# Optimization experiments

Measured on AMD Instinct MI355X. Metric: run time of the kernel, lower is better.

Reference implementation:

```python
import jax, jax.numpy as jnp
import numpy as np

# Model config (matches init_kwargs)
D_MODEL = 1536
NUM_HEADS = 16
QUERY_GROUPS = 4
HEAD_DIM = D_MODEL // NUM_HEADS  # 96
HEADS_PER_GROUP = NUM_HEADS // QUERY_GROUPS
ROPE_THETA = 10000.0
B, T, GH, GW = 2, 16, 16, 16
S = GH * GW  # spatial patches per frame
QKV_OUT = NUM_HEADS * HEAD_DIM + 2 * QUERY_GROUPS * HEAD_DIM  # 2304


def setup_inputs() -> dict:
    key = jax.random.key(0)
    k1, k2, k3 = jax.random.split(key, 3)
    x = jax.random.normal(k1, (B, T, S, D_MODEL), dtype=jnp.float32)
    padding_mask = jnp.ones((B * T, S), dtype=jnp.int32)
    # nn.Linear weights stored as [out, in]; y = x @ W.T
    w_qkv = jax.random.normal(k2, (QKV_OUT, D_MODEL), dtype=jnp.float32) * (1.0 / np.sqrt(D_MODEL))
    w_o = jax.random.normal(k3, (D_MODEL, D_MODEL), dtype=jnp.float32) * (1.0 / np.sqrt(D_MODEL))
    return {"x": x, "padding_mask": padding_mask, "w_qkv": w_qkv, "w_o": w_o}


def _rot_half(seg, cos, sin):
    # seg: [..., d]; half-split rotary rotation
    d = seg.shape[-1] // 2
    x1, x2 = seg[..., :d], seg[..., d:]
    return jnp.concatenate([x1 * cos - x2 * sin, x1 * sin + x2 * cos], axis=-1)


def _cos_sin(pos, seg_dim):
    # pos: [L] -> cos/sin [L, seg_dim//2]
    inv_freq = 1.0 / (ROPE_THETA ** (jnp.arange(seg_dim // 2, dtype=jnp.float32) * 2.0 / seg_dim))
    ang = pos.astype(jnp.float32)[:, None] * inv_freq[None, :]
    return jnp.cos(ang), jnp.sin(ang)


def _apply_rope3d(x):
    # x: [B*T, S, heads, HEAD_DIM]; head_dim split equally over (t, h, w) axes
    seg = HEAD_DIM // 3  # 32
    t_pos = jnp.tile(jnp.arange(T), B)            # [B*T] temporal index per attention-batch row
    h_pos = jnp.repeat(jnp.arange(GH), GW)        # [S]
    w_pos = jnp.tile(jnp.arange(GW), GH)          # [S]
    ct, st = _cos_sin(t_pos, seg)  # [B*T, seg/2]
    ch, sh = _cos_sin(h_pos, seg)  # [S, seg/2]
    cw, sw = _cos_sin(w_pos, seg)
    xt = _rot_half(x[..., :seg], ct[:, None, None, :], st[:, None, None, :])
    xh = _rot_half(x[..., seg:2 * seg], ch[None, :, None, :], sh[None, :, None, :])
    xw = _rot_half(x[..., 2 * seg:], cw[None, :, None, :], sw[None, :, None, :])
    return jnp.concatenate([xt, xh, xw], axis=-1)


def reference(x, padding_mask, w_qkv, w_o):
    # Spatial attention mode: [B, T, S, D] -> [B*T, S, D]
    xs = x.reshape(B * T, S, D_MODEL)
    qkv = jnp.einsum('bsd,od->bso', xs, w_qkv)  # [B*T, S, QKV_OUT]
    q_end = NUM_HEADS * HEAD_DIM
    k_end = q_end + QUERY_GROUPS * HEAD_DIM
    q = qkv[..., :q_end].reshape(B * T, S, NUM_HEADS, HEAD_DIM)
    k = qkv[..., q_end:k_end].reshape(B * T, S, QUERY_GROUPS, HEAD_DIM)
    v = qkv[..., k_end:].reshape(B * T, S, QUERY_GROUPS, HEAD_DIM)
    # RoPE3D on q and k
    q = _apply_rope3d(q)
    k = _apply_rope3d(k)
    # GQA: extend kv heads to num_heads (repeat_interleave)
    k = jnp.repeat(k, HEADS_PER_GROUP, axis=2)  # [B*T, S, NUM_HEADS, HEAD_DIM]
    v = jnp.repeat(v, HEADS_PER_GROUP, axis=2)
    scale = 1.0 / np.sqrt(HEAD_DIM)
    scores = jnp.einsum('bqhd,bkhd->bhqk', q, k) * scale  # [B*T, H, S, S]
    mask = (padding_mask != 0)[:, None, None, :]  # [B*T, 1, 1, S], True = attend
    scores = jnp.where(mask, scores, jnp.float32(-1e9))
    probs = jax.nn.softmax(scores, axis=-1)
    attn = jnp.einsum('bhqk,bkhd->bqhd', probs, v).reshape(B * T, S, D_MODEL)
    out = jnp.einsum('bsd,od->bso', attn, w_o)
    return out.reshape(B, T, S, D_MODEL)
```

## Files before the change

### kernel.cpp

```cpp
#include <hip/hip_runtime.h>
#include <hip/hip_bf16.h>
#include <stdint.h>

typedef __attribute__((ext_vector_type(8))) short short8;
typedef __attribute__((ext_vector_type(4))) float f32x4;
typedef __attribute__((ext_vector_type(4))) float f4;
typedef __attribute__((ext_vector_type(4))) short s4;

typedef __attribute__((address_space(1))) const void gvoid_t;
typedef __attribute__((address_space(3))) void lvoid_t;

__device__ __forceinline__ void gload_lds16(const void* g, void* l) {
  __builtin_amdgcn_global_load_lds((gvoid_t*)g, (lvoid_t*)l, 16, 0, 0);
}

__device__ __forceinline__ ushort f2b(float f) {
  union { float f; uint32_t u; } v; v.f = f;
  return (ushort)((v.u + 0x7fffu + ((v.u >> 16) & 1u)) >> 16);
}
__device__ __forceinline__ float b2f(ushort b) {
  union { uint32_t u; float f; } v; v.u = ((uint32_t)b) << 16;
  return v.f;
}

template <int N> __device__ __forceinline__ void wait_vmcnt();
template <> __device__ __forceinline__ void wait_vmcnt<0>() { asm volatile("s_waitcnt vmcnt(0)" ::: "memory"); }

__device__ __forceinline__ void wait_lgkm0() {
  asm volatile("s_waitcnt lgkmcnt(0)" ::: "memory");
  __builtin_amdgcn_sched_barrier(0);
}

__global__ void cvt_kernel(const float* __restrict__ in, ushort* __restrict__ out, int n4) {
  int i = blockIdx.x * 256 + threadIdx.x;
  if (i < n4) {
    f4 v = ((const f4*)in)[i];
    s4 o;
    o.x = (short)f2b(v.x); o.y = (short)f2b(v.y);
    o.z = (short)f2b(v.z); o.w = (short)f2b(v.w);
    ((s4*)out)[i] = o;
  }
}

template <int BN, typename OutT>
__global__ __launch_bounds__(512, 2) void gemm6(const ushort* __restrict__ A,
                                                const ushort* __restrict__ B,
                                                OutT* __restrict__ C,
                                                int N, int K) {
  constexpr int NF = BN / 32;
  constexpr int RB = BN / 2;
  constexpr int ABUF = 256 * 64;
  constexpr int BBUF = BN * 64;
  constexpr uint ABYTE = ABUF * 2;
  constexpr uint BBYTE = BBUF * 2;
  constexpr int BRND = BN / 64;
  constexpr int BTW = (BN % 64) / 8;

  __shared__ ushort As[2 * ABUF];
  __shared__ ushort Bs[2 * BBUF];

  const int tid = threadIdx.x;
  const int l = tid & 63, w = tid >> 6;
  const int wr = w >> 1, wc = w & 1;
  const int r16 = l & 15, kh = l >> 4;
  const int sc = (l & 7) ^ (l >> 3);
  const int srow = w * 8 + (l >> 3);

  const int xcd = blockIdx.x & 7;
  const int ii = blockIdx.x >> 3;
  const int bm = xcd * 4 + (ii & 3);
  const int bn = ii >> 2;
  const ushort* Ag = A + (size_t)bm * 256 * K;
  const ushort* Bg = B + (size_t)bn * BN * K;
  const int NT = K >> 6;

  const char* AsR = (const char*)As;
  const char* BsR = (const char*)Bs;
  const uint khsw = ((uint)kh * 16) ^ ((uint)(r16 & 7) * 16);
  const uint PA = (uint)(wr * 64 + r16) * 128 + khsw;
  const uint PB = (uint)(wc * RB + r16) * 128 + khsw;

  const ushort* ga[4];
  const ushort* gb[BRND];
  const ushort* gbt = nullptr;
#pragma unroll
  for (int i = 0; i < 4; ++i) ga[i] = Ag + (size_t)(i * 64 + srow) * K + sc * 8;
#pragma unroll
  for (int i = 0; i < BRND; ++i) gb[i] = Bg + (size_t)(i * 64 + srow) * K + sc * 8;
  if constexpr (BTW > 0) gbt = Bg + (size_t)(BRND * 64 + srow) * K + sc * 8;

#pragma unroll
  for (int i = 0; i < 4; ++i) gload_lds16(ga[i], As + i * 4096 + w * 512);
#pragma unroll
  for (int i = 0; i < BRND; ++i) gload_lds16(gb[i], Bs + i * 4096 + w * 512);
  if constexpr (BTW > 0) { if (w < BTW) gload_lds16(gbt, Bs + BRND * 4096 + w * 512); }
#pragma unroll
  for (int i = 0; i < 4; ++i) ga[i] += 64;
#pragma unroll
  for (int i = 0; i < BRND; ++i) gb[i] += 64;
  if constexpr (BTW > 0) gbt += 64;
  wait_vmcnt<0>();
  __builtin_amdgcn_s_barrier();

  f32x4 acc[4][NF] = {};
  short8 afr[4], bfr[NF];

  for (int u = 0; u < NT; ++u) {
    const int cur = u & 1;
    const uint aoff = cur ? ABYTE : 0u;
    const uint boff = cur ? BBYTE : 0u;
    ushort* An = As + (cur ^ 1) * ABUF;
    ushort* Bn = Bs + (cur ^ 1) * BBUF;
    const bool st = (u + 1 < NT);

    {
      const uint pa = PA + aoff, pb = PB + boff;
#pragma unroll
      for (int m = 0; m < 4; ++m)
        afr[m] = *(const short8*)(AsR + pa + m * 2048);
#pragma unroll
      for (int n = 0; n < NF; ++n)
        bfr[n] = *(const short8*)(BsR + pb + n * 2048);
    }
    if (st) {
#pragma unroll
      for (int i = 0; i < 4; ++i) gload_lds16(ga[i], An + i * 4096 + w * 512);
    }
    wait_lgkm0();
    __builtin_amdgcn_s_setprio(1);
#pragma unroll
    for (int m = 0; m < 4; ++m)
#pragma unroll
      for (int n = 0; n < NF; ++n)
        acc[m][n] = __builtin_amdgcn_mfma_f32_16x16x32_bf16(afr[m], bfr[n], acc[m][n], 0, 0, 0);
    __builtin_amdgcn_s_setprio(0);

    {
      const uint pa = (PA ^ 64u) + aoff, pb = (PB ^ 64u) + boff;
#pragma unroll
      for (int m = 0; m < 4; ++m)
        afr[m] = *(const short8*)(AsR + pa + m * 2048);
#pragma unroll
      for (int n = 0; n < NF; ++n)
        bfr[n] = *(const short8*)(BsR + pb + n * 2048);
    }
    if (st) {
#pragma unroll
      for (int i = 0; i < BRND; ++i) gload_lds16(gb[i], Bn + i * 4096 + w * 512);
      if constexpr (BTW > 0) { if (w < BTW) gload_lds16(gbt, Bn + BRND * 4096 + w * 512); }
    }
    wait_lgkm0();
    __builtin_amdgcn_s_setprio(1);
#pragma unroll
    for (int m = 0; m < 4; ++m)
#pragma unroll
      for (int n = 0; n < NF; ++n)
        acc[m][n] = __builtin_amdgcn_mfma_f32_16x16x32_bf16(afr[m], bfr[n], acc[m][n], 0, 0, 0);
    __builtin_amdgcn_s_setprio(0);

#pragma unroll
    for (int i = 0; i < 4; ++i) ga[i] += 64;
#pragma unroll
    for (int i = 0; i < BRND; ++i) gb[i] += 64;
    if constexpr (BTW > 0) gbt += 64;
    wait_vmcnt<0>();
    __builtin_amdgcn_s_barrier();
  }

  const int rowb = bm * 256 + wr * 64;
  const int colb = bn * BN + wc * RB;
#pragma unroll
  for (int m = 0; m < 4; ++m)
#pragma unroll
    for (int n = 0; n < NF; ++n)
#pragma unroll
      for (int r = 0; r < 4; ++r) {
        int row = rowb + m * 16 + kh * 4 + r;
        int col = colb + n * 16 + r16;
        float val = acc[m][n][r];
        if constexpr (sizeof(OutT) == 2) C[(size_t)row * N + col] = f2b(val);
        else                             C[(size_t)row * N + col] = val;
      }
}

__global__ void rope_tab_kernel(float2* __restrict__ tab) {
  int t = threadIdx.x;
  int pos = t >> 4, i = t & 15;
  float inv_freq = __expf(-(float)i * 0.5756462732485115f);
  float ang = (float)pos * inv_freq;
  float sn, c;
  __sincosf(ang, &sn, &c);
  tab[t] = make_float2(c, sn);
}

__global__ void rope_kernel(const ushort* __restrict__ qkv,
                            const float2* __restrict__ tab,
                            ushort* __restrict__ Qo, ushort* __restrict__ Ko,
                            ushort* __restrict__ Vt) {
  const int UNITS = 1344;
  int idx = blockIdx.x * 256 + threadIdx.x;
  if (idx >= 8192 * UNITS) return;
  int row = idx / UNITS;
  int unit = idx - row * UNITS;
  int bt = row >> 8, s = row & 255;
  const ushort* qr = qkv + (size_t)row * 2304;
  if (unit < 960) {
    int head, p;
    size_t srcoff;
    ushort* dst;
    if (unit < 768) {
      head = unit / 48; p = unit % 48;
      srcoff = (size_t)head * 96;
      dst = Qo + ((size_t)(bt * 16 + head) * 256 + s) * 96;
    } else {
      int u = unit - 768;
      head = u / 48; p = u % 48;
      srcoff = 1536 + (size_t)head * 96;
      dst = Ko + ((size_t)(bt * 4 + head) * 256 + s) * 96;
    }
    int seg = p >> 4, i = p & 15;
    int pos = (seg == 0) ? (bt & 15) : ((seg == 1) ? (s >> 4) : (s & 15));
    float2 cs = tab[pos * 16 + i];
    float c = cs.x, sn = cs.y;
    float x1 = b2f(qr[srcoff + seg * 32 + i]);
    float x2 = b2f(qr[srcoff + seg * 32 + i + 16]);
    dst[seg * 32 + i]      = f2b(x1 * c - x2 * sn);
    dst[seg * 32 + i + 16] = f2b(x1 * sn + x2 * c);
  } else {
    int u = unit - 960;
    int g = u / 96, d = u - g * 96;
    Vt[((size_t)(bt * 4 + g) * 96 + d) * 256 + s] = qr[1920 + (size_t)g * 96 + d];
  }
}

__global__ __launch_bounds__(512, 2) void attn2_kernel(
    const ushort* __restrict__ Q,
    const ushort* __restrict__ Kr,
    const ushort* __restrict__ Vt,
    const int* __restrict__ mask,
    ushort* __restrict__ Out) {
  __shared__ ushort Ks[256 * 104];
  __shared__ ushort Vs[96 * 264];
  __shared__ ushort Ps[8][16 * 136];
  __shared__ float Mb[256];

  const int b = blockIdx.x;
  const int qt = b & 1;
  const int g = (b >> 1) & 3;
  const int bt = b >> 3;
  const int t = threadIdx.x;
  const int l = t & 63, w = t >> 6;
  const int r16 = l & 15, kh = l >> 4;
  const int h = g * 4 + (w >> 1);
  const int qc = w & 1;

  const ushort* Kp = Kr + (size_t)(bt * 4 + g) * 256 * 96;
  const ushort* Vp = Vt + (size_t)(bt * 4 + g) * 96 * 256;

  {
    int r = t >> 1, ch = t & 1;
#pragma unroll
    for (int j = 0; j < 6; ++j)
      *(short8*)(&Ks[r * 104 + ch * 48 + j * 8]) =
          *(const short8*)(Kp + (size_t)r * 96 + ch * 48 + j * 8);
  }
#pragma unroll
  for (int i = 0; i < 6; ++i) {
    int c = t + i * 512;
    int vr = c >> 5, vc = c & 31;
    *(short8*)(&Vs[vr * 264 + vc * 8]) =
        *(const short8*)(Vp + (size_t)vr * 256 + vc * 8);
  }
  if (t < 256) Mb[t] = mask[bt * 256 + t] ? 0.0f : -1.0e9f;
  __syncthreads();

  const ushort* Qp = Q + ((size_t)(bt * 16 + h) * 256 + qt * 128 + qc * 64) * 96;
  ushort* Pw = &Ps[w][0];
  const float scale = 0.10206207261596575f;

#pragma unroll
  for (int mp = 0; mp < 2; ++mp) {
    const int qb = mp * 32;

    short8 qfA[3], qfB[3];
#pragma unroll
    for (int kc = 0; kc < 3; ++kc) {
      qfA[kc] = *(const short8*)(Qp + (size_t)(qb + r16) * 96 + kc * 32 + kh * 8);
      qfB[kc] = *(const short8*)(Qp + (size_t)(qb + 16 + r16) * 96 + kc * 32 + kh * 8);
    }

    f32x4 scA[16] = {}, scB[16] = {};
#pragma unroll
    for (int f = 0; f < 16; ++f) {
#pragma unroll
      for (int kc = 0; kc < 3; ++kc) {
        short8 kf = *(const short8*)(&Ks[(f * 16 + r16) * 104 + kc * 32 + kh * 8]);
        scA[f] = __builtin_amdgcn_mfma_f32_16x16x32_bf16(qfA[kc], kf, scA[f], 0, 0, 0);
        scB[f] = __builtin_amdgcn_mfma_f32_16x16x32_bf16(qfB[kc], kf, scB[f], 0, 0, 0);
      }
    }

#pragma unroll
    for (int f = 0; f < 16; ++f) {
      float mb = Mb[f * 16 + r16];
#pragma unroll
      for (int r = 0; r < 4; ++r) {
        scA[f][r] = scA[f][r] * scale + mb;
        scB[f][r] = scB[f][r] * scale + mb;
      }
    }

    float invA[4], invB[4];
#pragma unroll
    for (int reg = 0; reg < 4; ++reg) {
      float mxA = -3.0e38f, mxB = -3.0e38f;
#pragma unroll
      for (int f = 0; f < 16; ++f) { mxA = fmaxf(mxA, scA[f][reg]); mxB = fmaxf(mxB, scB[f][reg]); }
      for (int o = 8; o >= 1; o >>= 1) { mxA = fmaxf(mxA, __shfl_xor(mxA, o, 64)); mxB = fmaxf(mxB, __shfl_xor(mxB, o, 64)); }
      float smA = 0.f, smB = 0.f;
#pragma unroll
      for (int f = 0; f < 16; ++f) {
        float pA = __expf(scA[f][reg] - mxA);
        float pB = __expf(scB[f][reg] - mxB);
        scA[f][reg] = pA; scB[f][reg] = pB;
        smA += pA; smB += pB;
      }
      for (int o = 8; o >= 1; o >>= 1) { smA += __shfl_xor(smA, o, 64); smB += __shfl_xor(smB, o, 64); }
      invA[reg] = 1.0f / smA;
      invB[reg] = 1.0f / smB;
    }

    short8 pfA[8], pfB[8];
#pragma unroll
    for (int ck = 0; ck < 2; ++ck) {
#pragma unroll
      for (int f = 0; f < 8; ++f)
#pragma unroll
        for (int reg = 0; reg < 4; ++reg)
          Pw[(kh * 4 + reg) * 136 + f * 16 + r16] = f2b(scA[ck * 8 + f][reg]);
#pragma unroll
      for (int kc = 0; kc < 4; ++kc)
        pfA[ck * 4 + kc] = *(const short8*)(&Pw[r16 * 136 + kc * 32 + kh * 8]);
    }
#pragma unroll
    for (int ck = 0; ck < 2; ++ck) {
#pragma unroll
      for (int f = 0; f < 8; ++f)
#pragma unroll
        for (int reg = 0; reg < 4; ++reg)
          Pw[(kh * 4 + reg) * 136 + f * 16 + r16] = f2b(scB[ck * 8 + f][reg]);
#pragma unroll
      for (int kc = 0; kc < 4; ++kc)
        pfB[ck * 4 + kc] = *(const short8*)(&Pw[r16 * 136 + kc * 32 + kh * 8]);
    }

    f32x4 oA[6] = {}, oB[6] = {};
#pragma unroll
    for (int dt = 0; dt < 6; ++dt) {
#pragma unroll
      for (int kc = 0; kc < 8; ++kc) {
        short8 vf = *(const short8*)(&Vs[(dt * 16 + r16) * 264 + kc * 32 + kh * 8]);
        oA[dt] = __builtin_amdgcn_mfma_f32_16x16x32_bf16(pfA[kc], vf, oA[dt], 0, 0, 0);
        oB[dt] = __builtin_amdgcn_mfma_f32_16x16x32_bf16(pfB[kc], vf, oB[dt], 0, 0, 0);
      }
    }

    const int rbase = bt * 256 + qt * 128 + qc * 64 + qb;
#pragma unroll
    for (int dt = 0; dt < 6; ++dt)
#pragma unroll
      for (int reg = 0; reg < 4; ++reg) {
        int col = h * 96 + dt * 16 + r16;
        Out[(size_t)(rbase + kh * 4 + reg) * 1536 + col]      = f2b(oA[dt][reg] * invA[reg]);
        Out[(size_t)(rbase + 16 + kh * 4 + reg) * 1536 + col] = f2b(oB[dt][reg] * invB[reg]);
      }
  }
}

extern "C" void kernel_launch(void* const* d_in, const int* in_sizes, int n_in,
                              void* d_out, int out_size, void* d_ws, size_t ws_size,
                              hipStream_t stream) {
  const float* x     = (const float*)d_in[0];
  const int* pmask   = (const int*)d_in[1];
  const float* w_qkv = (const float*)d_in[2];
  const float* w_o   = (const float*)d_in[3];
  float* out = (float*)d_out;

  char* ws = (char*)d_ws;
  ushort* Xb  = (ushort*)(ws + 0);
  ushort* Wq  = (ushort*)(ws + 25165824);
  ushort* Wo  = (ushort*)(ws + 32243712);
  ushort* QKV = (ushort*)(ws + 36962304);
  ushort* Qr  = (ushort*)(ws + 74711040);
  ushort* Kr  = (ushort*)(ws + 99876864);
  ushort* Vt  = (ushort*)(ws + 106168320);
  float2* Tab = (float2*)(ws + 112459776);
  ushort* Attn = Xb;

  cvt_kernel<<<3145728 / 256, 256, 0, stream>>>(x, Xb, 3145728);
  cvt_kernel<<<884736 / 256, 256, 0, stream>>>(w_qkv, Wq, 884736);
  cvt_kernel<<<589824 / 256, 256, 0, stream>>>(w_o, Wo, 589824);
  rope_tab_kernel<<<1, 256, 0, stream>>>(Tab);

  gemm6<288, ushort><<<256, 512, 0, stream>>>(Xb, Wq, QKV, 2304, 1536);

  rope_kernel<<<(8192 * 1344) / 256, 256, 0, stream>>>(QKV, Tab, Qr, Kr, Vt);

  attn2_kernel<<<256, 512, 0, stream>>>(Qr, Kr, Vt, pmask, Attn);

  gemm6<192, float><<<256, 512, 0, stream>>>(Attn, Wo, out, 1536, 1536);
}
```

Measured before the change: 168.2 us.

## Load A fragments directly from global into registers, keep only B in LDS

The GEMM kernel no longer stages the A tile in shared memory. Each wave now loads its own A fragments straight from global memory into registers, prefetched one k-step ahead, and only B is double-buffered in LDS. The vmcnt waits are partial so that the A prefetches can stay in flight across the barrier. This removes A's LDS traffic and shared-memory footprint, at the cost of less coalesced global reads for A and more registers per thread.

```diff
diff --git a/kernel.cpp b/kernel.cpp
--- a/kernel.cpp
+++ b/kernel.cpp
@@ -25,11 +25,9 @@
 
 template <int N> __device__ __forceinline__ void wait_vmcnt();
 template <> __device__ __forceinline__ void wait_vmcnt<0>() { asm volatile("s_waitcnt vmcnt(0)" ::: "memory"); }
-
-__device__ __forceinline__ void wait_lgkm0() {
-  asm volatile("s_waitcnt lgkmcnt(0)" ::: "memory");
-  __builtin_amdgcn_sched_barrier(0);
-}
+template <> __device__ __forceinline__ void wait_vmcnt<8>() { asm volatile("s_waitcnt vmcnt(8)" ::: "memory"); }
+
+#define SB_VMEM() __builtin_amdgcn_sched_barrier(0x30F)
 
 __global__ void cvt_kernel(const float* __restrict__ in, ushort* __restrict__ out, int n4) {
   int i = blockIdx.x * 256 + threadIdx.x;
@@ -43,20 +41,17 @@
 }
 
 template <int BN, typename OutT>
-__global__ __launch_bounds__(512, 2) void gemm6(const ushort* __restrict__ A,
-                                                const ushort* __restrict__ B,
-                                                OutT* __restrict__ C,
-                                                int N, int K) {
+__global__ __launch_bounds__(512, 2) void gemm8k(const ushort* __restrict__ A,
+                                                 const ushort* __restrict__ B,
+                                                 OutT* __restrict__ C,
+                                                 int N, int K) {
   constexpr int NF = BN / 32;
   constexpr int RB = BN / 2;
-  constexpr int ABUF = 256 * 64;
   constexpr int BBUF = BN * 64;
-  constexpr uint ABYTE = ABUF * 2;
   constexpr uint BBYTE = BBUF * 2;
   constexpr int BRND = BN / 64;
   constexpr int BTW = (BN % 64) / 8;
 
-  __shared__ ushort As[2 * ABUF];
   __shared__ ushort Bs[2 * BBUF];
 
   const int tid = threadIdx.x;
@@ -74,96 +69,85 @@
   const ushort* Bg = B + (size_t)bn * BN * K;
   const int NT = K >> 6;
 
-  const char* AsR = (const char*)As;
   const char* BsR = (const char*)Bs;
   const uint khsw = ((uint)kh * 16) ^ ((uint)(r16 & 7) * 16);
-  const uint PA = (uint)(wr * 64 + r16) * 128 + khsw;
   const uint PB = (uint)(wc * RB + r16) * 128 + khsw;
 
-  const ushort* ga[4];
-  const ushort* gb[BRND];
-  const ushort* gbt = nullptr;
-#pragma unroll
-  for (int i = 0; i < 4; ++i) ga[i] = Ag + (size_t)(i * 64 + srow) * K + sc * 8;
-#pragma unroll
-  for (int i = 0; i < BRND; ++i) gb[i] = Bg + (size_t)(i * 64 + srow) * K + sc * 8;
-  if constexpr (BTW > 0) gbt = Bg + (size_t)(BRND * 64 + srow) * K + sc * 8;
-
-#pragma unroll
-  for (int i = 0; i < 4; ++i) gload_lds16(ga[i], As + i * 4096 + w * 512);
-#pragma unroll
-  for (int i = 0; i < BRND; ++i) gload_lds16(gb[i], Bs + i * 4096 + w * 512);
-  if constexpr (BTW > 0) { if (w < BTW) gload_lds16(gbt, Bs + BRND * 4096 + w * 512); }
-#pragma unroll
-  for (int i = 0; i < 4; ++i) ga[i] += 64;
-#pragma unroll
-  for (int i = 0; i < BRND; ++i) gb[i] += 64;
-  if constexpr (BTW > 0) gbt += 64;
-  wait_vmcnt<0>();
+  const ushort* Ab = Ag + (size_t)(wr * 64 + r16) * K + kh * 8;
+  const ushort* Bb = Bg + (size_t)srow * K + sc * 8;
+
+  short8 a0[4], a1[4];
+
+#pragma unroll
+  for (int i = 0; i < BRND; ++i) gload_lds16(Bb + (size_t)i * 64 * K, Bs + i * 4096 + w * 512);
+  if constexpr (BTW > 0) { if (w < BTW) gload_lds16(Bb + (size_t)BRND * 64 * K, Bs + BRND * 4096 + w * 512); }
+  SB_VMEM();
+#pragma unroll
+  for (int m = 0; m < 4; ++m) a0[m] = *(const short8*)(Ab + m * 16 * K);
+  SB_VMEM();
+#pragma unroll
+  for (int m = 0; m < 4; ++m) a1[m] = *(const short8*)(Ab + m * 16 * K + 32);
+  SB_VMEM();
+  wait_vmcnt<8>();
   __builtin_amdgcn_s_barrier();
 
   f32x4 acc[4][NF] = {};
-  short8 afr[4], bfr[NF];
 
   for (int u = 0; u < NT; ++u) {
     const int cur = u & 1;
-    const uint aoff = cur ? ABYTE : 0u;
     const uint boff = cur ? BBYTE : 0u;
-    ushort* An = As + (cur ^ 1) * ABUF;
     ushort* Bn = Bs + (cur ^ 1) * BBUF;
     const bool st = (u + 1 < NT);
-
+    const int kt1 = (u + 1) * 64;
+
+    if (st) {
+#pragma unroll
+      for (int i = 0; i < BRND; ++i)
+        gload_lds16(Bb + (size_t)i * 64 * K + kt1, Bn + i * 4096 + w * 512);
+      if constexpr (BTW > 0) {
+        if (w < BTW) gload_lds16(Bb + (size_t)BRND * 64 * K + kt1, Bn + BRND * 4096 + w * 512);
+      }
+    }
+    SB_VMEM();
     {
-      const uint pa = PA + aoff, pb = PB + boff;
+      short8 bfr[NF];
+#pragma unroll
+      for (int n = 0; n < NF; ++n)
+        bfr[n] = *(const short8*)(BsR + PB + boff + n * 2048);
+      __builtin_amdgcn_s_setprio(1);
 #pragma unroll
       for (int m = 0; m < 4; ++m)
-        afr[m] = *(const short8*)(AsR + pa + m * 2048);
+#pragma unroll
+        for (int n = 0; n < NF; ++n)
+          acc[m][n] = __builtin_amdgcn_mfma_f32_16x16x32_bf16(a0[m], bfr[n], acc[m][n], 0, 0, 0);
+      __builtin_amdgcn_s_setprio(0);
+    }
+    if (st) {
+#pragma unroll
+      for (int m = 0; m < 4; ++m) a0[m] = *(const short8*)(Ab + m * 16 * K + kt1);
+    }
+    SB_VMEM();
+
+    {
+      short8 bfr[NF];
 #pragma unroll
       for (int n = 0; n < NF; ++n)
-        bfr[n] = *(const short8*)(BsR + pb + n * 2048);
+        bfr[n] = *(const short8*)(BsR + ((PB ^ 64u) + boff) + n * 2048);
+      __builtin_amdgcn_s_setprio(1);
+#pragma unroll
+      for (int m = 0; m < 4; ++m)
+#pragma unroll
+        for (int n = 0; n < NF; ++n)
+          acc[m][n] = __builtin_amdgcn_mfma_f32_16x16x32_bf16(a1[m], bfr[n], acc[m][n], 0, 0, 0);
+      __builtin_amdgcn_s_setprio(0);
     }
     if (st) {
 #pragma unroll
-      for (int i = 0; i < 4; ++i) gload_lds16(ga[i], An + i * 4096 + w * 512);
-    }
-    wait_lgkm0();
-    __builtin_amdgcn_s_setprio(1);
-#pragma unroll
-    for (int m = 0; m < 4; ++m)
-#pragma unroll
-      for (int n = 0; n < NF; ++n)
-        acc[m][n] = __builtin_amdgcn_mfma_f32_16x16x32_bf16(afr[m], bfr[n], acc[m][n], 0, 0, 0);
-    __builtin_amdgcn_s_setprio(0);
-
-    {
-      const uint pa = (PA ^ 64u) + aoff, pb = (PB ^ 64u) + boff;
-#pragma unroll
-      for (int m = 0; m < 4; ++m)
-        afr[m] = *(const short8*)(AsR + pa + m * 2048);
-#pragma unroll
-      for (int n = 0; n < NF; ++n)
-        bfr[n] = *(const short8*)(BsR + pb + n * 2048);
-    }
-    if (st) {
-#pragma unroll
-      for (int i = 0; i < BRND; ++i) gload_lds16(gb[i], Bn + i * 4096 + w * 512);
-      if constexpr (BTW > 0) { if (w < BTW) gload_lds16(gbt, Bn + BRND * 4096 + w * 512); }
-    }
-    wait_lgkm0();
-    __builtin_amdgcn_s_setprio(1);
-#pragma unroll
-    for (int m = 0; m < 4; ++m)
-#pragma unroll
-      for (int n = 0; n < NF; ++n)
-        acc[m][n] = __builtin_amdgcn_mfma_f32_16x16x32_bf16(afr[m], bfr[n], acc[m][n], 0, 0, 0);
-    __builtin_amdgcn_s_setprio(0);
-
-#pragma unroll
-    for (int i = 0; i < 4; ++i) ga[i] += 64;
-#pragma unroll
-    for (int i = 0; i < BRND; ++i) gb[i] += 64;
-    if constexpr (BTW > 0) gbt += 64;
-    wait_vmcnt<0>();
+      for (int m = 0; m < 4; ++m) a1[m] = *(const short8*)(Ab + m * 16 * K + kt1 + 32);
+    }
+    SB_VMEM();
+
+    if (st) wait_vmcnt<8>(); else wait_vmcnt<0>();
     __builtin_amdgcn_s_barrier();
   }
 
@@ -402,11 +386,11 @@
   cvt_kernel<<<589824 / 256, 256, 0, stream>>>(w_o, Wo, 589824);
   rope_tab_kernel<<<1, 256, 0, stream>>>(Tab);
 
-  gemm6<288, ushort><<<256, 512, 0, stream>>>(Xb, Wq, QKV, 2304, 1536);
+  gemm8k<288, ushort><<<256, 512, 0, stream>>>(Xb, Wq, QKV, 2304, 1536);
 
   rope_kernel<<<(8192 * 1344) / 256, 256, 0, stream>>>(QKV, Tab, Qr, Kr, Vt);
 
   attn2_kernel<<<256, 512, 0, stream>>>(Qr, Kr, Vt, pmask, Attn);
 
-  gemm6<192, float><<<256, 512, 0, stream>>>(Attn, Wo, out, 1536, 1536);
-}
+  gemm8k<192, float><<<256, 512, 0, stream>>>(Attn, Wo, out, 1536, 1536);
+}
```

After: 211.0 us. 1.25x slower.

## Fuse RoPE into QKV GEMM epilogue, merge prep kernels, add V transpose

Applied to the files above, without the earlier changes.

Moves the 3D rotary embedding into the QKV GEMM epilogue. The kernel reads the partner half-segment from neighbouring accumulators, or from the other wave via LDS, and writes Q/K/V straight into head-major layout. This removes the bf16 QKV intermediate round-trip and the large per-element rope kernel. The three fp32→bf16 conversions and the rope table build are merged into one launch, and a small vectorised kernel handles the V transpose. The trade-offs are a heavier, scattered-store epilogue (stride-96 writes) and an extra LDS exchange plus sync at the GEMM tail.

```diff
diff --git a/kernel.cpp b/kernel.cpp
--- a/kernel.cpp
+++ b/kernel.cpp
@@ -30,16 +30,33 @@
   asm volatile("s_waitcnt lgkmcnt(0)" ::: "memory");
   __builtin_amdgcn_sched_barrier(0);
 }
-
-__global__ void cvt_kernel(const float* __restrict__ in, ushort* __restrict__ out, int n4) {
-  int i = blockIdx.x * 256 + threadIdx.x;
-  if (i < n4) {
-    f4 v = ((const f4*)in)[i];
-    s4 o;
-    o.x = (short)f2b(v.x); o.y = (short)f2b(v.y);
-    o.z = (short)f2b(v.z); o.w = (short)f2b(v.w);
-    ((s4*)out)[i] = o;
-  }
+__device__ __forceinline__ void barrier_fence() {
+  asm volatile("s_barrier" ::: "memory");
+}
+
+__global__ void prep_kernel(const float* __restrict__ x, const float* __restrict__ wq,
+                            const float* __restrict__ wo,
+                            ushort* __restrict__ Xb, ushort* __restrict__ Wq,
+                            ushort* __restrict__ Wo, float2* __restrict__ tab) {
+  int b = blockIdx.x, tid = threadIdx.x;
+  const float* in; ushort* out; int i;
+  if (b < 12288)      { in = x;  out = Xb; i = b * 256 + tid; }
+  else if (b < 15744) { in = wq; out = Wq; i = (b - 12288) * 256 + tid; }
+  else if (b < 18048) { in = wo; out = Wo; i = (b - 15744) * 256 + tid; }
+  else {
+    int pos = tid >> 4, fi = tid & 15;
+    float inv_freq = __expf(-(float)fi * 0.5756462732485115f);
+    float ang = (float)pos * inv_freq;
+    float sn, c;
+    __sincosf(ang, &sn, &c);
+    tab[tid] = make_float2(c, sn);
+    return;
+  }
+  f4 v = ((const f4*)in)[i];
+  s4 o;
+  o.x = (short)f2b(v.x); o.y = (short)f2b(v.y);
+  o.z = (short)f2b(v.z); o.w = (short)f2b(v.w);
+  ((s4*)out)[i] = o;
 }
 
 template <int BN, typename OutT>
@@ -100,7 +117,7 @@
   for (int i = 0; i < BRND; ++i) gb[i] += 64;
   if constexpr (BTW > 0) gbt += 64;
   wait_vmcnt<0>();
-  __builtin_amdgcn_s_barrier();
+  barrier_fence();
 
   f32x4 acc[4][NF] = {};
   short8 afr[4], bfr[NF];
@@ -116,11 +133,9 @@
     {
       const uint pa = PA + aoff, pb = PB + boff;
 #pragma unroll
-      for (int m = 0; m < 4; ++m)
-        afr[m] = *(const short8*)(AsR + pa + m * 2048);
-#pragma unroll
-      for (int n = 0; n < NF; ++n)
-        bfr[n] = *(const short8*)(BsR + pb + n * 2048);
+      for (int m = 0; m < 4; ++m) afr[m] = *(const short8*)(AsR + pa + m * 2048);
+#pragma unroll
+      for (int n = 0; n < NF; ++n) bfr[n] = *(const short8*)(BsR + pb + n * 2048);
     }
     if (st) {
 #pragma unroll
@@ -138,11 +153,9 @@
     {
       const uint pa = (PA ^ 64u) + aoff, pb = (PB ^ 64u) + boff;
 #pragma unroll
-      for (int m = 0; m < 4; ++m)
-        afr[m] = *(const short8*)(AsR + pa + m * 2048);
-#pragma unroll
-      for (int n = 0; n < NF; ++n)
-        bfr[n] = *(const short8*)(BsR + pb + n * 2048);
+      for (int m = 0; m < 4; ++m) afr[m] = *(const short8*)(AsR + pa + m * 2048);
+#pragma unroll
+      for (int n = 0; n < NF; ++n) bfr[n] = *(const short8*)(BsR + pb + n * 2048);
     }
     if (st) {
 #pragma unroll
@@ -164,7 +177,7 @@
     for (int i = 0; i < BRND; ++i) gb[i] += 64;
     if constexpr (BTW > 0) gbt += 64;
     wait_vmcnt<0>();
-    __builtin_amdgcn_s_barrier();
+    barrier_fence();
   }
 
   const int rowb = bm * 256 + wr * 64;
@@ -183,53 +196,204 @@
       }
 }
 
-__global__ void rope_tab_kernel(float2* __restrict__ tab) {
-  int t = threadIdx.x;
-  int pos = t >> 4, i = t & 15;
-  float inv_freq = __expf(-(float)i * 0.5756462732485115f);
-  float ang = (float)pos * inv_freq;
-  float sn, c;
-  __sincosf(ang, &sn, &c);
-  tab[t] = make_float2(c, sn);
-}
-
-__global__ void rope_kernel(const ushort* __restrict__ qkv,
-                            const float2* __restrict__ tab,
-                            ushort* __restrict__ Qo, ushort* __restrict__ Ko,
-                            ushort* __restrict__ Vt) {
-  const int UNITS = 1344;
-  int idx = blockIdx.x * 256 + threadIdx.x;
-  if (idx >= 8192 * UNITS) return;
-  int row = idx / UNITS;
-  int unit = idx - row * UNITS;
-  int bt = row >> 8, s = row & 255;
-  const ushort* qr = qkv + (size_t)row * 2304;
-  if (unit < 960) {
-    int head, p;
-    size_t srcoff;
+__global__ __launch_bounds__(512, 2) void gemm6r(const ushort* __restrict__ A,
+                                                 const ushort* __restrict__ B,
+                                                 ushort* __restrict__ Qr,
+                                                 ushort* __restrict__ Kr,
+                                                 ushort* __restrict__ Vr,
+                                                 const float2* __restrict__ Tab,
+                                                 int K) {
+  constexpr int BN = 288;
+  constexpr int NF = 9;
+  constexpr int RB = 144;
+  constexpr int ABUF = 256 * 64;
+  constexpr int BBUF = BN * 64;
+  constexpr uint ABYTE = ABUF * 2;
+  constexpr uint BBYTE = BBUF * 2;
+  constexpr int BRND = 4;
+  constexpr int BTW = 4;
+
+  __shared__ ushort As[2 * ABUF];
+  __shared__ ushort Bs[2 * BBUF];
+
+  const int tid = threadIdx.x;
+  const int l = tid & 63, w = tid >> 6;
+  const int wr = w >> 1, wc = w & 1;
+  const int r16 = l & 15, kh = l >> 4;
+  const int sc = (l & 7) ^ (l >> 3);
+  const int srow = w * 8 + (l >> 3);
+
+  const int xcd = blockIdx.x & 7;
+  const int ii = blockIdx.x >> 3;
+  const int bm = xcd * 4 + (ii & 3);
+  const int bn = ii >> 2;
+  const ushort* Ag = A + (size_t)bm * 256 * K;
+  const ushort* Bg = B + (size_t)bn * BN * K;
+  const int NT = K >> 6;
+
+  const char* AsR = (const char*)As;
+  const char* BsR = (const char*)Bs;
+  const uint khsw = ((uint)kh * 16) ^ ((uint)(r16 & 7) * 16);
+  const uint PA = (uint)(wr * 64 + r16) * 128 + khsw;
+  const uint PB = (uint)(wc * RB + r16) * 128 + khsw;
+
+  const ushort* ga[4];
+  const ushort* gb[BRND];
+  const ushort* gbt;
+#pragma unroll
+  for (int i = 0; i < 4; ++i) ga[i] = Ag + (size_t)(i * 64 + srow) * K + sc * 8;
+#pragma unroll
+  for (int i = 0; i < BRND; ++i) gb[i] = Bg + (size_t)(i * 64 + srow) * K + sc * 8;
+  gbt = Bg + (size_t)(BRND * 64 + srow) * K + sc * 8;
+
+#pragma unroll
+  for (int i = 0; i < 4; ++i) gload_lds16(ga[i], As + i * 4096 + w * 512);
+#pragma unroll
+  for (int i = 0; i < BRND; ++i) gload_lds16(gb[i], Bs + i * 4096 + w * 512);
+  if (w < BTW) gload_lds16(gbt, Bs + BRND * 4096 + w * 512);
+#pragma unroll
+  for (int i = 0; i < 4; ++i) ga[i] += 64;
+#pragma unroll
+  for (int i = 0; i < BRND; ++i) gb[i] += 64;
+  gbt += 64;
+  wait_vmcnt<0>();
+  barrier_fence();
+
+  f32x4 acc[4][NF] = {};
+  short8 afr[4], bfr[NF];
+
+  for (int u = 0; u < NT; ++u) {
+    const int cur = u & 1;
+    const uint aoff = cur ? ABYTE : 0u;
+    const uint boff = cur ? BBYTE : 0u;
+    ushort* An = As + (cur ^ 1) * ABUF;
+    ushort* Bn = Bs + (cur ^ 1) * BBUF;
+    const bool st = (u + 1 < NT);
+
+    {
+      const uint pa = PA + aoff, pb = PB + boff;
+#pragma unroll
+      for (int m = 0; m < 4; ++m) afr[m] = *(const short8*)(AsR + pa + m * 2048);
+#pragma unroll
+      for (int n = 0; n < NF; ++n) bfr[n] = *(const short8*)(BsR + pb + n * 2048);
+    }
+    if (st) {
+#pragma unroll
+      for (int i = 0; i < 4; ++i) gload_lds16(ga[i], An + i * 4096 + w * 512);
+    }
+    wait_lgkm0();
+    __builtin_amdgcn_s_setprio(1);
+#pragma unroll
+    for (int m = 0; m < 4; ++m)
+#pragma unroll
+      for (int n = 0; n < NF; ++n)
+        acc[m][n] = __builtin_amdgcn_mfma_f32_16x16x32_bf16(afr[m], bfr[n], acc[m][n], 0, 0, 0);
+    __builtin_amdgcn_s_setprio(0);
+
+    {
+      const uint pa = (PA ^ 64u) + aoff, pb = (PB ^ 64u) + boff;
+#pragma unroll
+      for (int m = 0; m < 4; ++m) afr[m] = *(const short8*)(AsR + pa + m * 2048);
+#pragma unroll
+      for (int n = 0; n < NF; ++n) bfr[n] = *(const short8*)(BsR + pb + n * 2048);
+    }
+    if (st) {
+#pragma unroll
+      for (int i = 0; i < BRND; ++i) gload_lds16(gb[i], Bn + i * 4096 + w * 512);
+      if (w < BTW) gload_lds16(gbt, Bn + BRND * 4096 + w * 512);
+    }
+    wait_lgkm0();
+    __builtin_amdgcn_s_setprio(1);
+#pragma unroll
+    for (int m = 0; m < 4; ++m)
+#pragma unroll
+      for (int n = 0; n < NF; ++n)
+        acc[m][n] = __builtin_amdgcn_mfma_f32_16x16x32_bf16(afr[m], bfr[n], acc[m][n], 0, 0, 0);
+    __builtin_amdgcn_s_setprio(0);
+
+#pragma unroll
+    for (int i = 0; i < 4; ++i) ga[i] += 64;
+#pragma unroll
+    for (int i = 0; i < BRND; ++i) gb[i] += 64;
+    gbt += 64;
+    wait_vmcnt<0>();
+    barrier_fence();
+  }
+
+  float* Xc = (float*)As;
+  const int myN = wc ? 0 : 8;
+#pragma unroll
+  for (int m = 0; m < 4; ++m)
+#pragma unroll
+    for (int r = 0; r < 4; ++r)
+      Xc[(((w * 4 + m) * 16) + kh * 4 + r) * 16 + r16] = acc[m][myN][r];
+  __syncthreads();
+  float xp[4][4];
+#pragma unroll
+  for (int m = 0; m < 4; ++m)
+#pragma unroll
+    for (int r = 0; r < 4; ++r)
+      xp[m][r] = Xc[((((w ^ 1) * 4 + m) * 16) + kh * 4 + r) * 16 + r16];
+
+  float c0, s0;
+  { float2 t = Tab[(bm & 15) * 16 + r16]; c0 = t.x; s0 = t.y; }
+  float c1[4], s1[4], c2[4], s2[4];
+#pragma unroll
+  for (int m = 0; m < 4; ++m) { float2 t = Tab[(wr * 4 + m) * 16 + r16]; c1[m] = t.x; s1[m] = t.y; }
+#pragma unroll
+  for (int r = 0; r < 4; ++r) { float2 t = Tab[(kh * 4 + r) * 16 + r16]; c2[r] = t.x; s2[r] = t.y; }
+
+#pragma unroll
+  for (int n = 0; n < NF; ++n) {
+    const int colb_n = bn * 288 + wc * 144 + n * 16;
+    const int q6 = (3 * wc + n) % 6;
+    const int seg = q6 >> 1, hi = q6 & 1;
+    const int head = 3 * bn + wc + (3 * wc + n) / 6;
+    const bool isV = colb_n >= 1920;
+    const bool isK = (colb_n >= 1536) && !isV;
     ushort* dst;
-    if (unit < 768) {
-      head = unit / 48; p = unit % 48;
-      srcoff = (size_t)head * 96;
-      dst = Qo + ((size_t)(bt * 16 + head) * 256 + s) * 96;
-    } else {
-      int u = unit - 768;
-      head = u / 48; p = u % 48;
-      srcoff = 1536 + (size_t)head * 96;
-      dst = Ko + ((size_t)(bt * 4 + head) * 256 + s) * 96;
-    }
-    int seg = p >> 4, i = p & 15;
-    int pos = (seg == 0) ? (bt & 15) : ((seg == 1) ? (s >> 4) : (s & 15));
-    float2 cs = tab[pos * 16 + i];
-    float c = cs.x, sn = cs.y;
-    float x1 = b2f(qr[srcoff + seg * 32 + i]);
-    float x2 = b2f(qr[srcoff + seg * 32 + i + 16]);
-    dst[seg * 32 + i]      = f2b(x1 * c - x2 * sn);
-    dst[seg * 32 + i + 16] = f2b(x1 * sn + x2 * c);
-  } else {
-    int u = unit - 960;
-    int g = u / 96, d = u - g * 96;
-    Vt[((size_t)(bt * 4 + g) * 96 + d) * 256 + s] = qr[1920 + (size_t)g * 96 + d];
+    if (isV)       dst = Vr + ((size_t)(bm * 4 + (head - 20)) * 256) * 96 + 16 * q6 + r16;
+    else if (isK)  dst = Kr + ((size_t)(bm * 4 + (head - 16)) * 256) * 96 + 16 * q6 + r16;
+    else           dst = Qr + ((size_t)(bm * 16 + head) * 256) * 96 + 16 * q6 + r16;
+#pragma unroll
+    for (int m = 0; m < 4; ++m)
+#pragma unroll
+      for (int r = 0; r < 4; ++r) {
+        const int s = wr * 64 + m * 16 + kh * 4 + r;
+        const float val = acc[m][n][r];
+        float outv;
+        if (isV) {
+          outv = val;
+        } else {
+          float c, sn;
+          if (seg == 0)      { c = c0;    sn = s0;    }
+          else if (seg == 1) { c = c1[m]; sn = s1[m]; }
+          else               { c = c2[r]; sn = s2[r]; }
+          const float part = (n == myN) ? xp[m][r] : acc[m][n + (hi ? -1 : 1)][r];
+          outv = hi ? (part * sn + val * c) : (val * c - part * sn);
+        }
+        dst[(size_t)s * 96] = f2b(outv);
+      }
+  }
+}
+
+__global__ void vtrans_kernel(const ushort* __restrict__ Vr, ushort* __restrict__ Vt) {
+  int tau = blockIdx.x * 256 + threadIdx.x;
+  int slice = tau / 384;
+  int rem = tau - slice * 384;
+  int dt = rem >> 5;
+  int st = rem & 31;
+  const ushort* src = Vr + (size_t)slice * 24576 + (size_t)(st * 8) * 96 + dt * 8;
+  ushort* dst = Vt + (size_t)slice * 24576 + (size_t)(dt * 8) * 256 + st * 8;
+  short8 rr[8];
+#pragma unroll
+  for (int j = 0; j < 8; ++j) rr[j] = *(const short8*)(src + (size_t)j * 96);
+#pragma unroll
+  for (int jj = 0; jj < 8; ++jj) {
+    short8 oo;
+#pragma unroll
+    for (int j = 0; j < 8; ++j) oo[j] = rr[j][jj];
+    *(short8*)(dst + (size_t)jj * 256) = oo;
   }
 }
 
@@ -390,21 +554,18 @@
   ushort* Xb  = (ushort*)(ws + 0);
   ushort* Wq  = (ushort*)(ws + 25165824);
   ushort* Wo  = (ushort*)(ws + 32243712);
-  ushort* QKV = (ushort*)(ws + 36962304);
+  ushort* Vr  = (ushort*)(ws + 36962304);
   ushort* Qr  = (ushort*)(ws + 74711040);
   ushort* Kr  = (ushort*)(ws + 99876864);
   ushort* Vt  = (ushort*)(ws + 106168320);
   float2* Tab = (float2*)(ws + 112459776);
   ushort* Attn = Xb;
 
-  cvt_kernel<<<3145728 / 256, 256, 0, stream>>>(x, Xb, 3145728);
-  cvt_kernel<<<884736 / 256, 256, 0, stream>>>(w_qkv, Wq, 884736);
-  cvt_kernel<<<589824 / 256, 256, 0, stream>>>(w_o, Wo, 589824);
-  rope_tab_kernel<<<1, 256, 0, stream>>>(Tab);
-
-  gemm6<288, ushort><<<256, 512, 0, stream>>>(Xb, Wq, QKV, 2304, 1536);
-
-  rope_kernel<<<(8192 * 1344) / 256, 256, 0, stream>>>(QKV, Tab, Qr, Kr, Vt);
+  prep_kernel<<<18049, 256, 0, stream>>>(x, w_qkv, w_o, Xb, Wq, Wo, Tab);
+
+  gemm6r<<<256, 512, 0, stream>>>(Xb, Wq, Qr, Kr, Vr, Tab, 1536);
+
+  vtrans_kernel<<<192, 256, 0, stream>>>(Vr, Vt);
 
   attn2_kernel<<<256, 512, 0, stream>>>(Qr, Kr, Vt, pmask, Attn);
 
```

Measured after the change: 215.9 us. 1.28x slower.

## Fuse RoPE and V transpose into attention; merge conversion kernels into one launch

Applied to the files above, without the earlier changes.

Removes the separate rope kernel. The attention kernel now reads Q, K and V straight from the QKV buffer, applies RoPE to K while staging it into LDS, applies RoPE to Q fragments in registers using a cross-lane shuffle, and transposes V on its LDS store. The three fp32-to-bf16 conversions and the rope table are merged into a single prep launch. This saves the Q/K/V intermediate round trip through global memory and several launches. In exchange it adds strided global reads, scalar transposing LDS stores, and drops the attention kernel's launch bounds to one block per SM.

```diff
diff --git a/kernel.cpp b/kernel.cpp
--- a/kernel.cpp
+++ b/kernel.cpp
@@ -30,16 +30,33 @@
   asm volatile("s_waitcnt lgkmcnt(0)" ::: "memory");
   __builtin_amdgcn_sched_barrier(0);
 }
-
-__global__ void cvt_kernel(const float* __restrict__ in, ushort* __restrict__ out, int n4) {
-  int i = blockIdx.x * 256 + threadIdx.x;
-  if (i < n4) {
-    f4 v = ((const f4*)in)[i];
-    s4 o;
-    o.x = (short)f2b(v.x); o.y = (short)f2b(v.y);
-    o.z = (short)f2b(v.z); o.w = (short)f2b(v.w);
-    ((s4*)out)[i] = o;
-  }
+__device__ __forceinline__ void barrier_fence() {
+  asm volatile("s_barrier" ::: "memory");
+}
+
+__global__ void prep_kernel(const float* __restrict__ x, const float* __restrict__ wq,
+                            const float* __restrict__ wo,
+                            ushort* __restrict__ Xb, ushort* __restrict__ Wq,
+                            ushort* __restrict__ Wo, float2* __restrict__ tab) {
+  int b = blockIdx.x, tid = threadIdx.x;
+  const float* in; ushort* out; int i;
+  if (b < 12288)      { in = x;  out = Xb; i = b * 256 + tid; }
+  else if (b < 15744) { in = wq; out = Wq; i = (b - 12288) * 256 + tid; }
+  else if (b < 18048) { in = wo; out = Wo; i = (b - 15744) * 256 + tid; }
+  else {
+    int pos = tid >> 4, fi = tid & 15;
+    float inv_freq = __expf(-(float)fi * 0.5756462732485115f);
+    float ang = (float)pos * inv_freq;
+    float sn, c;
+    __sincosf(ang, &sn, &c);
+    tab[tid] = make_float2(c, sn);
+    return;
+  }
+  f4 v = ((const f4*)in)[i];
+  s4 o;
+  o.x = (short)f2b(v.x); o.y = (short)f2b(v.y);
+  o.z = (short)f2b(v.z); o.w = (short)f2b(v.w);
+  ((s4*)out)[i] = o;
 }
 
 template <int BN, typename OutT>
@@ -100,7 +117,7 @@
   for (int i = 0; i < BRND; ++i) gb[i] += 64;
   if constexpr (BTW > 0) gbt += 64;
   wait_vmcnt<0>();
-  __builtin_amdgcn_s_barrier();
+  barrier_fence();
 
   f32x4 acc[4][NF] = {};
   short8 afr[4], bfr[NF];
@@ -116,11 +133,9 @@
     {
       const uint pa = PA + aoff, pb = PB + boff;
 #pragma unroll
-      for (int m = 0; m < 4; ++m)
-        afr[m] = *(const short8*)(AsR + pa + m * 2048);
-#pragma unroll
-      for (int n = 0; n < NF; ++n)
-        bfr[n] = *(const short8*)(BsR + pb + n * 2048);
+      for (int m = 0; m < 4; ++m) afr[m] = *(const short8*)(AsR + pa + m * 2048);
+#pragma unroll
+      for (int n = 0; n < NF; ++n) bfr[n] = *(const short8*)(BsR + pb + n * 2048);
     }
     if (st) {
 #pragma unroll
@@ -138,11 +153,9 @@
     {
       const uint pa = (PA ^ 64u) + aoff, pb = (PB ^ 64u) + boff;
 #pragma unroll
-      for (int m = 0; m < 4; ++m)
-        afr[m] = *(const short8*)(AsR + pa + m * 2048);
-#pragma unroll
-      for (int n = 0; n < NF; ++n)
-        bfr[n] = *(const short8*)(BsR + pb + n * 2048);
+      for (int m = 0; m < 4; ++m) afr[m] = *(const short8*)(AsR + pa + m * 2048);
+#pragma unroll
+      for (int n = 0; n < NF; ++n) bfr[n] = *(const short8*)(BsR + pb + n * 2048);
     }
     if (st) {
 #pragma unroll
@@ -164,7 +177,7 @@
     for (int i = 0; i < BRND; ++i) gb[i] += 64;
     if constexpr (BTW > 0) gbt += 64;
     wait_vmcnt<0>();
-    __builtin_amdgcn_s_barrier();
+    barrier_fence();
   }
 
   const int rowb = bm * 256 + wr * 64;
@@ -183,66 +196,36 @@
       }
 }
 
-__global__ void rope_tab_kernel(float2* __restrict__ tab) {
-  int t = threadIdx.x;
-  int pos = t >> 4, i = t & 15;
-  float inv_freq = __expf(-(float)i * 0.5756462732485115f);
-  float ang = (float)pos * inv_freq;
-  float sn, c;
-  __sincosf(ang, &sn, &c);
-  tab[t] = make_float2(c, sn);
-}
-
-__global__ void rope_kernel(const ushort* __restrict__ qkv,
-                            const float2* __restrict__ tab,
-                            ushort* __restrict__ Qo, ushort* __restrict__ Ko,
-                            ushort* __restrict__ Vt) {
-  const int UNITS = 1344;
-  int idx = blockIdx.x * 256 + threadIdx.x;
-  if (idx >= 8192 * UNITS) return;
-  int row = idx / UNITS;
-  int unit = idx - row * UNITS;
-  int bt = row >> 8, s = row & 255;
-  const ushort* qr = qkv + (size_t)row * 2304;
-  if (unit < 960) {
-    int head, p;
-    size_t srcoff;
-    ushort* dst;
-    if (unit < 768) {
-      head = unit / 48; p = unit % 48;
-      srcoff = (size_t)head * 96;
-      dst = Qo + ((size_t)(bt * 16 + head) * 256 + s) * 96;
-    } else {
-      int u = unit - 768;
-      head = u / 48; p = u % 48;
-      srcoff = 1536 + (size_t)head * 96;
-      dst = Ko + ((size_t)(bt * 4 + head) * 256 + s) * 96;
-    }
-    int seg = p >> 4, i = p & 15;
-    int pos = (seg == 0) ? (bt & 15) : ((seg == 1) ? (s >> 4) : (s & 15));
-    float2 cs = tab[pos * 16 + i];
-    float c = cs.x, sn = cs.y;
-    float x1 = b2f(qr[srcoff + seg * 32 + i]);
-    float x2 = b2f(qr[srcoff + seg * 32 + i + 16]);
-    dst[seg * 32 + i]      = f2b(x1 * c - x2 * sn);
-    dst[seg * 32 + i + 16] = f2b(x1 * sn + x2 * c);
-  } else {
-    int u = unit - 960;
-    int g = u / 96, d = u - g * 96;
-    Vt[((size_t)(bt * 4 + g) * 96 + d) * 256 + s] = qr[1920 + (size_t)g * 96 + d];
-  }
-}
-
-__global__ __launch_bounds__(512, 2) void attn2_kernel(
-    const ushort* __restrict__ Q,
-    const ushort* __restrict__ Kr,
-    const ushort* __restrict__ Vt,
+__device__ __forceinline__ short8 shfl_xor32(short8 v) {
+  union { short8 s; int i[4]; } a, b;
+  a.s = v;
+#pragma unroll
+  for (int q = 0; q < 4; ++q) b.i[q] = __shfl_xor(a.i[q], 32, 64);
+  return b.s;
+}
+__device__ __forceinline__ short8 rope_frag(short8 v, int pos, int kh, const float2* Tb) {
+  short8 p = shfl_xor32(v);
+  const float sgn = (kh < 2) ? -1.0f : 1.0f;
+  const int ib = pos * 16 + (kh & 1) * 8;
+  short8 o;
+#pragma unroll
+  for (int j = 0; j < 8; ++j) {
+    float2 cs = Tb[ib + j];
+    o[j] = (short)f2b(b2f((ushort)v[j]) * cs.x + sgn * b2f((ushort)p[j]) * cs.y);
+  }
+  return o;
+}
+
+__global__ __launch_bounds__(512, 1) void attn3_kernel(
+    const ushort* __restrict__ QKV,
     const int* __restrict__ mask,
+    const float2* __restrict__ Tab,
     ushort* __restrict__ Out) {
   __shared__ ushort Ks[256 * 104];
   __shared__ ushort Vs[96 * 264];
   __shared__ ushort Ps[8][16 * 136];
   __shared__ float Mb[256];
+  __shared__ float2 Tb[256];
 
   const int b = blockIdx.x;
   const int qt = b & 1;
@@ -253,40 +236,111 @@
   const int r16 = l & 15, kh = l >> 4;
   const int h = g * 4 + (w >> 1);
   const int qc = w & 1;
-
-  const ushort* Kp = Kr + (size_t)(bt * 4 + g) * 256 * 96;
-  const ushort* Vp = Vt + (size_t)(bt * 4 + g) * 96 * 256;
+  const int t0 = bt & 15;
+
+  if (t < 256) { Tb[t] = Tab[t]; Mb[t] = mask[bt * 256 + t] ? 0.0f : -1.0e9f; }
+  __syncthreads();
 
   {
-    int r = t >> 1, ch = t & 1;
-#pragma unroll
-    for (int j = 0; j < 6; ++j)
-      *(short8*)(&Ks[r * 104 + ch * 48 + j * 8]) =
-          *(const short8*)(Kp + (size_t)r * 96 + ch * 48 + j * 8);
-  }
+    const int r = t >> 1, ch = t & 1;
+    const ushort* src = QKV + (size_t)(bt * 256 + r) * 2304 + 1536 + g * 96;
+    const int p1 = r >> 4, p2 = r & 15;
+    if (ch == 0) {
+      short8 v0 = *(const short8*)(src + 0);
+      short8 v1 = *(const short8*)(src + 8);
+      short8 v2 = *(const short8*)(src + 16);
+      short8 v3 = *(const short8*)(src + 24);
+      short8 o0, o1, o2, o3;
+#pragma unroll
+      for (int j = 0; j < 8; ++j) {
+        float2 ca = Tb[t0 * 16 + j], cb = Tb[t0 * 16 + 8 + j];
+        float x1a = b2f((ushort)v0[j]), x2a = b2f((ushort)v2[j]);
+        float x1b = b2f((ushort)v1[j]), x2b = b2f((ushort)v3[j]);
+        o0[j] = (short)f2b(x1a * ca.x - x2a * ca.y);
+        o1[j] = (short)f2b(x1b * cb.x - x2b * cb.y);
+        o2[j] = (short)f2b(x1a * ca.y + x2a * ca.x);
+        o3[j] = (short)f2b(x1b * cb.y + x2b * cb.x);
+      }
+      *(short8*)(&Ks[r * 104 + 0])  = o0;
+      *(short8*)(&Ks[r * 104 + 8])  = o1;
+      *(short8*)(&Ks[r * 104 + 16]) = o2;
+      *(short8*)(&Ks[r * 104 + 24]) = o3;
+      v0 = *(const short8*)(src + 32);
+      v1 = *(const short8*)(src + 40);
+      v2 = *(const short8*)(src + 48);
+      v3 = *(const short8*)(src + 56);
+#pragma unroll
+      for (int j = 0; j < 8; ++j) {
+        float2 ca = Tb[p1 * 16 + j], cb = Tb[p1 * 16 + 8 + j];
+        float x1a = b2f((ushort)v0[j]), x2a = b2f((ushort)v2[j]);
+        float x1b = b2f((ushort)v1[j]), x2b = b2f((ushort)v3[j]);
+        o0[j] = (short)f2b(x1a * ca.x - x2a * ca.y);
+        o1[j] = (short)f2b(x1b * cb.x - x2b * cb.y);
+        o2[j] = (short)f2b(x1a * ca.y + x2a * ca.x);
+        o3[j] = (short)f2b(x1b * cb.y + x2b * cb.x);
+      }
+      *(short8*)(&Ks[r * 104 + 32]) = o0;
+      *(short8*)(&Ks[r * 104 + 40]) = o1;
+      *(short8*)(&Ks[r * 104 + 48]) = o2;
+      *(short8*)(&Ks[r * 104 + 56]) = o3;
+    } else {
+      short8 v0 = *(const short8*)(src + 64);
+      short8 v1 = *(const short8*)(src + 72);
+      short8 v2 = *(const short8*)(src + 80);
+      short8 v3 = *(const short8*)(src + 88);
+      short8 o0, o1, o2, o3;
+#pragma unroll
+      for (int j = 0; j < 8; ++j) {
+        float2 ca = Tb[p2 * 16 + j], cb = Tb[p2 * 16 + 8 + j];
+        float x1a = b2f((ushort)v0[j]), x2a = b2f((ushort)v2[j]);
+        float x1b = b2f((ushort)v1[j]), x2b = b2f((ushort)v3[j]);
+        o0[j] = (short)f2b(x1a * ca.x - x2a * ca.y);
+        o1[j] = (short)f2b(x1b * cb.x - x2b * cb.y);
+        o2[j] = (short)f2b(x1a * ca.y + x2a * ca.x);
+        o3[j] = (short)f2b(x1b * cb.y + x2b * cb.x);
+      }
+      *(short8*)(&Ks[r * 104 + 64]) = o0;
+      *(short8*)(&Ks[r * 104 + 72]) = o1;
+      *(short8*)(&Ks[r * 104 + 80]) = o2;
+      *(short8*)(&Ks[r * 104 + 88]) = o3;
+    }
+  }
+
 #pragma unroll
   for (int i = 0; i < 6; ++i) {
     int c = t + i * 512;
-    int vr = c >> 5, vc = c & 31;
-    *(short8*)(&Vs[vr * 264 + vc * 8]) =
-        *(const short8*)(Vp + (size_t)vr * 256 + vc * 8);
-  }
-  if (t < 256) Mb[t] = mask[bt * 256 + t] ? 0.0f : -1.0e9f;
+    int s = c / 12, dq = c - s * 12;
+    short8 vv = *(const short8*)(QKV + (size_t)(bt * 256 + s) * 2304 + 1920 + g * 96 + dq * 8);
+#pragma unroll
+    for (int j = 0; j < 8; ++j)
+      Vs[(dq * 8 + j) * 264 + s] = (ushort)vv[j];
+  }
   __syncthreads();
 
-  const ushort* Qp = Q + ((size_t)(bt * 16 + h) * 256 + qt * 128 + qc * 64) * 96;
+  const ushort* Qp = QKV + (size_t)(bt * 256 + qt * 128 + qc * 64) * 2304 + h * 96;
   ushort* Pw = &Ps[w][0];
   const float scale = 0.10206207261596575f;
 
 #pragma unroll
   for (int mp = 0; mp < 2; ++mp) {
     const int qb = mp * 32;
+    const int p1A = qt * 8 + qc * 4 + mp * 2;
+    const int p1B = p1A + 1;
 
     short8 qfA[3], qfB[3];
-#pragma unroll
-    for (int kc = 0; kc < 3; ++kc) {
-      qfA[kc] = *(const short8*)(Qp + (size_t)(qb + r16) * 96 + kc * 32 + kh * 8);
-      qfB[kc] = *(const short8*)(Qp + (size_t)(qb + 16 + r16) * 96 + kc * 32 + kh * 8);
+    {
+      short8 rA0 = *(const short8*)(Qp + (size_t)(qb + r16) * 2304 + 0 + kh * 8);
+      short8 rA1 = *(const short8*)(Qp + (size_t)(qb + r16) * 2304 + 32 + kh * 8);
+      short8 rA2 = *(const short8*)(Qp + (size_t)(qb + r16) * 2304 + 64 + kh * 8);
+      short8 rB0 = *(const short8*)(Qp + (size_t)(qb + 16 + r16) * 2304 + 0 + kh * 8);
+      short8 rB1 = *(const short8*)(Qp + (size_t)(qb + 16 + r16) * 2304 + 32 + kh * 8);
+      short8 rB2 = *(const short8*)(Qp + (size_t)(qb + 16 + r16) * 2304 + 64 + kh * 8);
+      qfA[0] = rope_frag(rA0, t0, kh, Tb);
+      qfA[1] = rope_frag(rA1, p1A, kh, Tb);
+      qfA[2] = rope_frag(rA2, r16, kh, Tb);
+      qfB[0] = rope_frag(rB0, t0, kh, Tb);
+      qfB[1] = rope_frag(rB1, p1B, kh, Tb);
+      qfB[2] = rope_frag(rB2, r16, kh, Tb);
     }
 
     f32x4 scA[16] = {}, scB[16] = {};
@@ -391,22 +445,14 @@
   ushort* Wq  = (ushort*)(ws + 25165824);
   ushort* Wo  = (ushort*)(ws + 32243712);
   ushort* QKV = (ushort*)(ws + 36962304);
-  ushort* Qr  = (ushort*)(ws + 74711040);
-  ushort* Kr  = (ushort*)(ws + 99876864);
-  ushort* Vt  = (ushort*)(ws + 106168320);
-  float2* Tab = (float2*)(ws + 112459776);
+  float2* Tab = (float2*)(ws + 74711040);
   ushort* Attn = Xb;
 
-  cvt_kernel<<<3145728 / 256, 256, 0, stream>>>(x, Xb, 3145728);
-  cvt_kernel<<<884736 / 256, 256, 0, stream>>>(w_qkv, Wq, 884736);
-  cvt_kernel<<<589824 / 256, 256, 0, stream>>>(w_o, Wo, 589824);
-  rope_tab_kernel<<<1, 256, 0, stream>>>(Tab);
+  prep_kernel<<<18049, 256, 0, stream>>>(x, w_qkv, w_o, Xb, Wq, Wo, Tab);
 
   gemm6<288, ushort><<<256, 512, 0, stream>>>(Xb, Wq, QKV, 2304, 1536);
 
-  rope_kernel<<<(8192 * 1344) / 256, 256, 0, stream>>>(QKV, Tab, Qr, Kr, Vt);
-
-  attn2_kernel<<<256, 512, 0, stream>>>(Qr, Kr, Vt, pmask, Attn);
+  attn3_kernel<<<256, 512, 0, stream>>>(QKV, pmask, Tab, Attn);
 
   gemm6<192, float><<<256, 512, 0, stream>>>(Attn, Wo, out, 1536, 1536);
 }
```

Result: faster. 147.0 us (-12.6%).
